# Kernel tuning notes

Measured on AMD Instinct MI355X. Metric: run time of the kernel, lower is better.

Reference implementation:

```python
import jax, jax.numpy as jnp
import numpy as np

N = 100000
F_IN = 128
HID = 64
N_CLS = 40
E = 1600000


def gcn_conv(x, src, dst, W, b, n_nodes):
    """PyG GCNConv: add self-loops, symmetric deg^{-1/2} normalization.

    Self-loop contribution handled analytically (norm_ii = 1/deg_i) so we
    never concatenate self-loop edges.
    """
    h = x @ W                                      # [N, out]
    # in-degree including self-loop
    deg = jax.ops.segment_sum(jnp.ones((src.shape[0],), x.dtype), dst,
                              num_segments=n_nodes) + 1.0
    dinv = jax.lax.rsqrt(deg)                      # deg^{-1/2}, [N]
    norm = dinv[src] * dinv[dst]                   # [E]
    msg = h[src] * norm[:, None]                   # [E, out] gather + scale
    agg = jax.ops.segment_sum(msg, dst, num_segments=n_nodes)
    return agg + h * (dinv * dinv)[:, None] + b


def setup_inputs() -> dict:
    key = jax.random.key(0)
    k1, k2, k3, k4, k5, k6 = jax.random.split(key, 6)
    x = jax.random.normal(k1, (N, F_IN), dtype=jnp.float32)
    edge_index = jax.random.randint(k2, (2, E), 0, N, dtype=jnp.int64)
    W1 = jax.random.normal(k3, (F_IN, HID), dtype=jnp.float32) / np.sqrt(F_IN)
    b1 = jnp.zeros((HID,), jnp.float32)
    W2 = jax.random.normal(k4, (HID, N_CLS), dtype=jnp.float32) / np.sqrt(HID)
    b2 = jnp.zeros((N_CLS,), jnp.float32)
    return {"x": x, "edge_index": edge_index, "W1": W1, "b1": b1,
            "W2": W2, "b2": b2}


def reference(x, edge_index, W1, b1, W2, b2):
    src, dst = edge_index[0], edge_index[1]
    h = jax.nn.relu(gcn_conv(x, src, dst, W1, b1, N))
    # dropout p=0.5 is identity at inference (training=False)
    out = gcn_conv(h, src, dst, W2, b2, N)
    return out
```

## Files before the change

kernel.cpp:

```cpp
#include <hip/hip_runtime.h>
#include <hip/hip_fp16.h>
#include <stdint.h>

#define NN    100000
#define FIN   128
#define HIDN  64
#define NCLS  40
#define NE    1600000
#define NBUCK ((NN + 255) / 256)
#define EPB   4096
#define NEB   ((NE + EPB - 1) / EPB)

typedef unsigned int uint32;
typedef __attribute__((ext_vector_type(8))) short short8v;
typedef __attribute__((ext_vector_type(4))) float f32x4;

static __device__ __forceinline__ unsigned short f2bf(float f) {
  uint32 u = __float_as_uint(f);
  u = (u + 0x7fffu + ((u >> 16) & 1u)) >> 16;
  return (unsigned short)u;
}
static __device__ __forceinline__ uint32 pack2(float lo, float hi) {
  return (uint32)f2bf(lo) | ((uint32)f2bf(hi) << 16);
}
static __device__ __forceinline__ float bf_lo(uint32 v) {
  return __uint_as_float(v << 16);
}
static __device__ __forceinline__ float bf_hi(uint32 v) {
  return __uint_as_float(v & 0xFFFF0000u);
}
static __device__ __forceinline__ float2 h2f2(uint32 w) {
  __half2 h = __builtin_bit_cast(__half2, w);
  return __half22float2(h);
}
static __device__ __forceinline__ f32x4 mfma_bf16(uint4 a, uint4 b, f32x4 c) {
  short8v av = __builtin_bit_cast(short8v, a);
  short8v bv = __builtin_bit_cast(short8v, b);
  return __builtin_amdgcn_mfma_f32_16x16x32_bf16(av, bv, c, 0, 0, 0);
}

static __device__ __forceinline__ int perm_col(int z) {
  return 4 * (z >> 3) + ((z & 7) >> 1) + 16 * (z & 1) + ((z >= 32) ? 16 : 0);
}

#define ACC8(v)                                                              \
  do {                                                                       \
    a[0] += bf_lo((v).x); a[1] += bf_hi((v).x);                              \
    a[2] += bf_lo((v).y); a[3] += bf_hi((v).y);                              \
    a[4] += bf_lo((v).z); a[5] += bf_hi((v).z);                              \
    a[6] += bf_lo((v).w); a[7] += bf_hi((v).w);                              \
  } while (0)

#define ACC8H(v)                                                             \
  do {                                                                       \
    float2 f0 = h2f2((v).x), f1 = h2f2((v).y);                               \
    float2 f2 = h2f2((v).z), f3 = h2f2((v).w);                               \
    a[0] += f0.x; a[1] += f0.y; a[2] += f1.x; a[3] += f1.y;                  \
    a[4] += f2.x; a[5] += f2.y; a[6] += f3.x; a[7] += f3.y;                  \
  } while (0)

__global__ __launch_bounds__(64) void wfrag_kernel(const float* __restrict__ W,
                                                   const float* __restrict__ b1,
                                                   const float* __restrict__ W2,
                                                   const unsigned int* __restrict__ raw,
                                                   uint4* __restrict__ wfrag,
                                                   uint4* __restrict__ w2frag,
                                                   float* __restrict__ b1p,
                                                   int* __restrict__ flag) {
  int bk = blockIdx.x;
  int tid = threadIdx.x;
  if (bk < 32) {
    int idx = bk * 64 + tid;
    int lane = idx & 63;
    int nr = (idx >> 6) & 3;
    int kr = (idx >> 8) & 3;
    int t  = idx >> 10;
    int n  = nr * 16 + (lane & 15);
    int k0 = kr * 32 + (lane >> 4) * 8;
    uint32 w[4];
#pragma unroll
    for (int j = 0; j < 4; ++j) {
      float a = W[(k0 + 2 * j) * HIDN + n];
      float b = W[(k0 + 2 * j + 1) * HIDN + n];
      uint32 ha = f2bf(a), hb = f2bf(b);
      if (t == 0) {
        w[j] = ha | (hb << 16);
      } else {
        float ra = a - __uint_as_float(ha << 16);
        float rb = b - __uint_as_float(hb << 16);
        w[j] = (uint32)f2bf(ra) | ((uint32)f2bf(rb) << 16);
      }
    }
    wfrag[idx] = make_uint4(w[0], w[1], w[2], w[3]);
  } else if (bk < 44) {
    int f = bk - 32;
    int t2 = f / 6;
    int kr = (f / 3) % 2;
    int nf = f % 3;
    int c  = nf * 16 + (tid & 15);
    int k0 = kr * 32 + (tid >> 4) * 8;
    uint32 w[4];
#pragma unroll
    for (int j = 0; j < 4; ++j) {
      float a = (c < NCLS) ? W2[perm_col(k0 + 2 * j) * NCLS + c] : 0.f;
      float b = (c < NCLS) ? W2[perm_col(k0 + 2 * j + 1) * NCLS + c] : 0.f;
      uint32 ha = f2bf(a), hb = f2bf(b);
      if (t2 == 0) {
        w[j] = ha | (hb << 16);
      } else {
        float ra = a - __uint_as_float(ha << 16);
        float rb = b - __uint_as_float(hb << 16);
        w[j] = (uint32)f2bf(ra) | ((uint32)f2bf(rb) << 16);
      }
    }
    w2frag[f * 64 + tid] = make_uint4(w[0], w[1], w[2], w[3]);
  } else {
    b1p[tid] = b1[perm_col(tid)];
    if (tid == 0) {
      int is64 = 1;
      for (int i = 0; i < 64; ++i)
        if (raw[2 * i + 1] != 0u) { is64 = 0; break; }
      *flag = is64;
    }
  }
}

__global__ __launch_bounds__(256) void passA_kernel(const void* __restrict__ eptr,
                                                    const int* __restrict__ flag,
                                                    int* __restrict__ mat) {
  __shared__ int cnt[NBUCK];
  int tid = threadIdx.x;
  for (int i = tid; i < NBUCK; i += 256) cnt[i] = 0;
  __syncthreads();
  int is64 = *flag;
  int base = blockIdx.x * EPB;
#pragma unroll
  for (int k = 0; k < EPB / 256; ++k) {
    int e = base + k * 256 + tid;
    if (e < NE) {
      int d = is64 ? (int)((const long long*)eptr)[e + NE]
                   : ((const int*)eptr)[e + NE];
      atomicAdd(&cnt[d >> 8], 1);
    }
  }
  __syncthreads();
  for (int i = tid; i < NBUCK; i += 256)
    mat[blockIdx.x * NBUCK + i] = cnt[i];
}

__global__ __launch_bounds__(512) void passB1_kernel(int* __restrict__ mat,
                                                     int* __restrict__ tot) {
  __shared__ int s[512];
  int b = blockIdx.x;
  int t = threadIdx.x;
  int v = (t < NEB) ? mat[t * NBUCK + b] : 0;
  s[t] = v;
  __syncthreads();
#pragma unroll
  for (int d = 1; d < 512; d <<= 1) {
    int u = (t >= d) ? s[t - d] : 0;
    __syncthreads();
    s[t] += u;
    __syncthreads();
  }
  if (t < NEB) mat[t * NBUCK + b] = s[t] - v;
  if (t == 511) tot[b] = s[511];
}

__global__ __launch_bounds__(512) void passB2_kernel(const int* __restrict__ tot,
                                                     int* __restrict__ bbase) {
  __shared__ int s[512];
  int i = threadIdx.x;
  int v = (i < NBUCK) ? tot[i] : 0;
  s[i] = v;
  __syncthreads();
#pragma unroll
  for (int d = 1; d < 512; d <<= 1) {
    int u = (i >= d) ? s[i - d] : 0;
    __syncthreads();
    s[i] += u;
    __syncthreads();
  }
  if (i < NBUCK) bbase[i] = s[i] - v;
  if (i == 511) bbase[NBUCK] = s[511];
}

__global__ __launch_bounds__(256) void passC_kernel(const void* __restrict__ eptr,
                                                    const int* __restrict__ flag,
                                                    const int* __restrict__ mat,
                                                    const int* __restrict__ bbase,
                                                    uint32* __restrict__ bbuf) {
  __shared__ int cur[NBUCK];
  int tid = threadIdx.x;
  for (int i = tid; i < NBUCK; i += 256)
    cur[i] = bbase[i] + mat[blockIdx.x * NBUCK + i];
  __syncthreads();
  int is64 = *flag;
  int base = blockIdx.x * EPB;
#pragma unroll
  for (int k = 0; k < EPB / 256; ++k) {
    int e = base + k * 256 + tid;
    if (e < NE) {
      int s, d;
      if (is64) {
        const long long* p = (const long long*)eptr;
        s = (int)p[e]; d = (int)p[e + NE];
      } else {
        const int* p = (const int*)eptr;
        s = p[e]; d = p[e + NE];
      }
      int slot = atomicAdd(&cur[d >> 8], 1);
      bbuf[slot] = (uint32)s | ((uint32)(d & 255) << 17);
    }
  }
}

__global__ __launch_bounds__(256) void build_kernel(const int* __restrict__ bbase,
                                                    const uint32* __restrict__ bbuf,
                                                    int* __restrict__ off,
                                                    float* __restrict__ dinv,
                                                    int* __restrict__ s_src) {
  __shared__ int hist[256];
  __shared__ int lofs[256];
  __shared__ int rank[256];
  int b = blockIdx.x, tid = threadIdx.x;
  int base = bbase[b];
  int count = bbase[b + 1] - base;
  const uint32* p = bbuf + base;
  hist[tid] = 0;
  __syncthreads();
  for (int i = tid; i < count; i += 256) atomicAdd(&hist[p[i] >> 17], 1);
  __syncthreads();
  int deg = hist[tid];
  lofs[tid] = deg;
  __syncthreads();
#pragma unroll
  for (int dd = 1; dd < 256; dd <<= 1) {
    int t = (tid >= dd) ? lofs[tid - dd] : 0;
    __syncthreads();
    lofs[tid] += t;
    __syncthreads();
  }
  int excl = lofs[tid] - deg;
  __syncthreads();
  lofs[tid] = excl;
  rank[tid] = 0;
  int n = b * 256 + tid;
  if (n < NN) {
    off[n] = base + excl;
    dinv[n] = rsqrtf((float)deg + 1.0f);
  }
  if (b == 0 && tid == 0) off[NN] = NE;
  __syncthreads();
  for (int i = tid; i < count; i += 256) {
    uint32 v = p[i];
    int dl = (int)(v >> 17);
    int s = (int)(v & 0x1FFFFu);
    int r = atomicAdd(&rank[dl], 1);
    s_src[base + lofs[dl] + r] = s;
  }
}

__global__ __launch_bounds__(256) void gemm1_kernel(const float* __restrict__ x,
                                                    const uint4* __restrict__ wfrag,
                                                    const float* __restrict__ dinv,
                                                    uint32* __restrict__ hs) {
  int wid = blockIdx.x * 4 + (threadIdx.x >> 6);
  if (wid >= NN / 32) return;
  int lane = threadIdx.x & 63;
  int l15 = lane & 15, lg = lane >> 4;
  int r0 = wid * 32;
  f32x4 acc[2][4];
#pragma unroll
  for (int mr = 0; mr < 2; ++mr)
#pragma unroll
    for (int nr = 0; nr < 4; ++nr) acc[mr][nr] = (f32x4)0.f;
  const float4* x4 = (const float4*)x;
#pragma unroll
  for (int kr = 0; kr < 4; ++kr) {
    uint4 ah[2], al[2];
#pragma unroll
    for (int mr = 0; mr < 2; ++mr) {
      int m = r0 + mr * 16 + l15;
      int q0 = m * 32 + kr * 8 + lg * 2;
      float4 u = x4[q0], v = x4[q0 + 1];
      float xs[8] = {u.x, u.y, u.z, u.w, v.x, v.y, v.z, v.w};
      uint32 hw[4], lw[4];
#pragma unroll
      for (int j = 0; j < 4; ++j) {
        float a0 = xs[2 * j], a1 = xs[2 * j + 1];
        uint32 h0 = f2bf(a0), h1 = f2bf(a1);
        float ra = a0 - __uint_as_float(h0 << 16);
        float rb = a1 - __uint_as_float(h1 << 16);
        hw[j] = h0 | (h1 << 16);
        lw[j] = (uint32)f2bf(ra) | ((uint32)f2bf(rb) << 16);
      }
      ah[mr] = make_uint4(hw[0], hw[1], hw[2], hw[3]);
      al[mr] = make_uint4(lw[0], lw[1], lw[2], lw[3]);
    }
#pragma unroll
    for (int nr = 0; nr < 4; ++nr) {
      uint4 bh = wfrag[(kr * 4 + nr) * 64 + lane];
      uint4 bl = wfrag[((4 + kr) * 4 + nr) * 64 + lane];
#pragma unroll
      for (int mr = 0; mr < 2; ++mr) {
        acc[mr][nr] = mfma_bf16(ah[mr], bh, acc[mr][nr]);
        acc[mr][nr] = mfma_bf16(al[mr], bh, acc[mr][nr]);
        acc[mr][nr] = mfma_bf16(ah[mr], bl, acc[mr][nr]);
      }
    }
  }
#pragma unroll
  for (int mr = 0; mr < 2; ++mr) {
    int rb = r0 + mr * 16 + 4 * lg;
    float4 dv = *(const float4*)&dinv[rb];
#pragma unroll
    for (int a = 0; a < 2; ++a) {
#pragma unroll
      for (int j = 0; j < 4; ++j) {
        float d = (&dv.x)[j];
        uint32 wv = pack2(acc[mr][2 * a][j] * d, acc[mr][2 * a + 1][j] * d);
        hs[(size_t)(rb + j) * 32 + a * 16 + l15] = wv;
      }
    }
  }
}

__global__ __launch_bounds__(256) void agg1_kernel(const int* __restrict__ off,
                                                   const int* __restrict__ s_src,
                                                   const uint4* __restrict__ hs4,
                                                   const float* __restrict__ dinv,
                                                   const float* __restrict__ b1p,
                                                   uint4* __restrict__ g) {
  int tid = threadIdx.x;
  int n = blockIdx.x * 32 + (tid >> 3);
  int hc = tid & 7;
  int j0 = off[n], j1 = off[n + 1];
  float a[8];
  {
    uint4 v = hs4[(size_t)n * 8 + hc];
    a[0] = bf_lo(v.x); a[1] = bf_hi(v.x); a[2] = bf_lo(v.y); a[3] = bf_hi(v.y);
    a[4] = bf_lo(v.z); a[5] = bf_hi(v.z); a[6] = bf_lo(v.w); a[7] = bf_hi(v.w);
  }
  int j = j0;
  for (; j + 3 < j1; j += 4) {
    int s0 = s_src[j], s1 = s_src[j + 1], s2 = s_src[j + 2], s3 = s_src[j + 3];
    uint4 v0 = hs4[(size_t)s0 * 8 + hc];
    uint4 v1 = hs4[(size_t)s1 * 8 + hc];
    uint4 v2 = hs4[(size_t)s2 * 8 + hc];
    uint4 v3 = hs4[(size_t)s3 * 8 + hc];
    ACC8(v0); ACC8(v1); ACC8(v2); ACC8(v3);
  }
  for (; j < j1; ++j) {
    uint4 v0 = hs4[(size_t)s_src[j] * 8 + hc];
    ACC8(v0);
  }
  float di = dinv[n];
  float4 b0 = *(const float4*)&b1p[hc * 8];
  float4 b4 = *(const float4*)&b1p[hc * 8 + 4];
  float r0 = di * fmaxf(a[0] * di + b0.x, 0.f);
  float r1 = di * fmaxf(a[1] * di + b0.y, 0.f);
  float r2 = di * fmaxf(a[2] * di + b0.z, 0.f);
  float r3 = di * fmaxf(a[3] * di + b0.w, 0.f);
  float r4 = di * fmaxf(a[4] * di + b4.x, 0.f);
  float r5 = di * fmaxf(a[5] * di + b4.y, 0.f);
  float r6 = di * fmaxf(a[6] * di + b4.z, 0.f);
  float r7 = di * fmaxf(a[7] * di + b4.w, 0.f);
  uint4 o;
  o.x = pack2(r0, r1); o.y = pack2(r2, r3);
  o.z = pack2(r4, r5); o.w = pack2(r6, r7);
  g[(size_t)n * 8 + hc] = o;
}

__global__ __launch_bounds__(256) void gemm2_kernel(const uint4* __restrict__ g4,
                                                    const uint4* __restrict__ w2frag,
                                                    unsigned short* __restrict__ y16) {
  int wid = blockIdx.x * 4 + (threadIdx.x >> 6);
  if (wid >= NN / 32) return;
  int lane = threadIdx.x & 63;
  int l15 = lane & 15, lg = lane >> 4;
  int r0 = wid * 32;
  f32x4 acc[2][3];
#pragma unroll
  for (int mr = 0; mr < 2; ++mr)
#pragma unroll
    for (int nf = 0; nf < 3; ++nf) acc[mr][nf] = (f32x4)0.f;
#pragma unroll
  for (int kr = 0; kr < 2; ++kr) {
    uint4 a0 = g4[(size_t)(r0 + l15) * 8 + kr * 4 + lg];
    uint4 a1 = g4[(size_t)(r0 + 16 + l15) * 8 + kr * 4 + lg];
#pragma unroll
    for (int nf = 0; nf < 3; ++nf) {
      uint4 bh = w2frag[(kr * 3 + nf) * 64 + lane];
      uint4 bl = w2frag[((2 + kr) * 3 + nf) * 64 + lane];
      acc[0][nf] = mfma_bf16(a0, bh, acc[0][nf]);
      acc[0][nf] = mfma_bf16(a0, bl, acc[0][nf]);
      acc[1][nf] = mfma_bf16(a1, bh, acc[1][nf]);
      acc[1][nf] = mfma_bf16(a1, bl, acc[1][nf]);
    }
  }
#pragma unroll
  for (int mr = 0; mr < 2; ++mr) {
#pragma unroll
    for (int nf = 0; nf < 3; ++nf) {
      int col = nf * 16 + l15;
      if (col < NCLS) {
#pragma unroll
        for (int j = 0; j < 4; ++j) {
          int row = r0 + mr * 16 + 4 * lg + j;
          __half h = __float2half(acc[mr][nf][j]);
          y16[(size_t)row * NCLS + col] = __builtin_bit_cast(unsigned short, h);
        }
      }
    }
  }
}

__global__ __launch_bounds__(256) void agg2y_kernel(const int* __restrict__ off,
                                                    const int* __restrict__ s_src,
                                                    const uint4* __restrict__ y4,
                                                    const float* __restrict__ dinv,
                                                    const float* __restrict__ b2,
                                                    float* __restrict__ out) {
  int T = blockIdx.x * 256 + threadIdx.x;
  int n = T / 5;
  int sub = T - n * 5;
  if (n >= NN) return;
  int j0 = off[n], j1 = off[n + 1];
  float a[8];
  {
    uint4 v = y4[(size_t)n * 5 + sub];
    float2 f0 = h2f2(v.x), f1 = h2f2(v.y), f2 = h2f2(v.z), f3 = h2f2(v.w);
    a[0] = f0.x; a[1] = f0.y; a[2] = f1.x; a[3] = f1.y;
    a[4] = f2.x; a[5] = f2.y; a[6] = f3.x; a[7] = f3.y;
  }
  int j = j0;
  for (; j + 3 < j1; j += 4) {
    int s0 = s_src[j], s1 = s_src[j + 1], s2 = s_src[j + 2], s3 = s_src[j + 3];
    uint4 v0 = y4[(size_t)s0 * 5 + sub];
    uint4 v1 = y4[(size_t)s1 * 5 + sub];
    uint4 v2 = y4[(size_t)s2 * 5 + sub];
    uint4 v3 = y4[(size_t)s3 * 5 + sub];
    ACC8H(v0); ACC8H(v1); ACC8H(v2); ACC8H(v3);
  }
  for (; j < j1; ++j) {
    uint4 v0 = y4[(size_t)s_src[j] * 5 + sub];
    ACC8H(v0);
  }
  float di = dinv[n];
  int c0 = sub * 8;
  float4 bb0 = *(const float4*)&b2[c0];
  float4 bb1 = *(const float4*)&b2[c0 + 4];
  float* op = &out[(size_t)n * NCLS + c0];
  *(float4*)op = make_float4(a[0] * di + bb0.x, a[1] * di + bb0.y,
                             a[2] * di + bb0.z, a[3] * di + bb0.w);
  *(float4*)(op + 4) = make_float4(a[4] * di + bb1.x, a[5] * di + bb1.y,
                                   a[6] * di + bb1.z, a[7] * di + bb1.w);
}

extern "C" void kernel_launch(void* const* d_in, const int* in_sizes, int n_in,
                              void* d_out, int out_size, void* d_ws, size_t ws_size,
                              hipStream_t stream) {
  const float* x  = (const float*)d_in[0];
  const void*  ei = d_in[1];
  const float* W1 = (const float*)d_in[2];
  const float* b1 = (const float*)d_in[3];
  const float* W2 = (const float*)d_in[4];
  const float* b2 = (const float*)d_in[5];
  float* out = (float*)d_out;

  char* w = (char*)d_ws;
  size_t off_b = 0;
  auto carve = [&](size_t bytes) -> void* {
    void* p = w + off_b;
    off_b = (off_b + bytes + 255) & ~(size_t)255;
    return p;
  };
  int*    mat    = (int*)   carve((size_t)NEB * NBUCK * 4);
  int*    tot    = (int*)   carve((size_t)NBUCK * 4);
  int*    bbase  = (int*)   carve((size_t)(NBUCK + 1) * 4);
  int*    offs   = (int*)   carve((size_t)(NN + 1) * 4);
  float*  dinv   = (float*) carve((size_t)NN * 4);
  int*    flag   = (int*)   carve(256);
  int*    s_src  = (int*)   carve((size_t)NE * 4);
  uint32* hs     = (uint32*)carve((size_t)NN * 32 * 4);
  uint4*  g      = (uint4*) carve((size_t)NN * 8 * 16);
  uint32* bbuf   = (uint32*)carve((size_t)NE * 4);
  uint4*  wfrag  = (uint4*) carve((size_t)2048 * 16);
  uint4*  w2frag = (uint4*) carve((size_t)768 * 16);
  float*  b1p    = (float*) carve((size_t)HIDN * 4);
  unsigned short* y16 = (unsigned short*)carve((size_t)NN * NCLS * 2);

  wfrag_kernel<<<45, 64, 0, stream>>>(W1, b1, W2, (const unsigned int*)ei,
                                      wfrag, w2frag, b1p, flag);
  passA_kernel<<<NEB, 256, 0, stream>>>(ei, flag, mat);
  passB1_kernel<<<NBUCK, 512, 0, stream>>>(mat, tot);
  passB2_kernel<<<1, 512, 0, stream>>>(tot, bbase);
  passC_kernel<<<NEB, 256, 0, stream>>>(ei, flag, mat, bbase, bbuf);
  build_kernel<<<NBUCK, 256, 0, stream>>>(bbase, bbuf, offs, dinv, s_src);
  gemm1_kernel<<<(NN / 32 + 3) / 4, 256, 0, stream>>>(x, wfrag, dinv, hs);
  agg1_kernel<<<NN / 32, 256, 0, stream>>>(offs, s_src, (const uint4*)hs, dinv, b1p, g);
  gemm2_kernel<<<(NN / 32 + 3) / 4, 256, 0, stream>>>(g, w2frag, y16);
  agg2y_kernel<<<(NN * 5 + 255) / 256, 256, 0, stream>>>(offs, s_src,
                                                         (const uint4*)y16, dinv, b2, out);
}
```

Before: 229.7 us.

## Fuse CSR build passes into one persistent kernel with grid barriers

Merges the five CSR construction kernels (bucket count, two scans, scatter, per-bucket sort) into a single kernel of NEB=391 blocks separated by software grid-wide barriers on an atomic counter reset by the weight-prep kernel. The goal is to remove four kernel launch gaps and tail effects in the short preprocessing phase. It relies on all 391 blocks being co-resident (true on a 256-CU GPU, but not guaranteed), and it serializes the single-block bucket scan behind a barrier that every block spins on.

Result: slower. 471.8 us (+105.4%).

```diff
diff --git a/kernel.cpp b/kernel.cpp
--- a/kernel.cpp
+++ b/kernel.cpp
@@ -66,7 +66,8 @@
                                                    uint4* __restrict__ wfrag,
                                                    uint4* __restrict__ w2frag,
                                                    float* __restrict__ b1p,
-                                                   int* __restrict__ flag) {
+                                                   int* __restrict__ flag,
+                                                   int* __restrict__ gbar) {
   int bk = blockIdx.x;
   int tid = threadIdx.x;
   if (bk < 32) {
@@ -121,82 +122,99 @@
       for (int i = 0; i < 64; ++i)
         if (raw[2 * i + 1] != 0u) { is64 = 0; break; }
       *flag = is64;
-    }
-  }
-}
-
-__global__ __launch_bounds__(256) void passA_kernel(const void* __restrict__ eptr,
-                                                    const int* __restrict__ flag,
-                                                    int* __restrict__ mat) {
-  __shared__ int cnt[NBUCK];
-  int tid = threadIdx.x;
-  for (int i = tid; i < NBUCK; i += 256) cnt[i] = 0;
+      *gbar = 0;
+    }
+  }
+}
+
+#define GRID_BAR(PH)                                                         \
+  do {                                                                       \
+    __syncthreads();                                                         \
+    if (threadIdx.x == 0) {                                                  \
+      __threadfence();                                                       \
+      __hip_atomic_fetch_add(gbar, 1, __ATOMIC_RELEASE,                      \
+                             __HIP_MEMORY_SCOPE_AGENT);                      \
+      while (__hip_atomic_load(gbar, __ATOMIC_ACQUIRE,                       \
+                               __HIP_MEMORY_SCOPE_AGENT) < NEB * (PH))       \
+        __builtin_amdgcn_s_sleep(2);                                         \
+      __threadfence();                                                       \
+    }                                                                        \
+    __syncthreads();                                                         \
+  } while (0)
+
+__global__ __launch_bounds__(256) void csr_kernel(const void* __restrict__ eptr,
+                                                  const int* __restrict__ flag,
+                                                  int* __restrict__ mat,
+                                                  int* __restrict__ tot,
+                                                  int* __restrict__ bbase,
+                                                  int* __restrict__ off,
+                                                  float* __restrict__ dinv,
+                                                  int* __restrict__ s_src,
+                                                  uint32* __restrict__ bbuf,
+                                                  int* __restrict__ gbar) {
+  __shared__ int smem[1024];
+  int b = blockIdx.x, tid = threadIdx.x;
+  int is64 = *flag;
+  int base = b * EPB;
+
+  for (int i = tid; i < NBUCK; i += 256) smem[i] = 0;
   __syncthreads();
-  int is64 = *flag;
-  int base = blockIdx.x * EPB;
 #pragma unroll
   for (int k = 0; k < EPB / 256; ++k) {
     int e = base + k * 256 + tid;
     if (e < NE) {
       int d = is64 ? (int)((const long long*)eptr)[e + NE]
                    : ((const int*)eptr)[e + NE];
-      atomicAdd(&cnt[d >> 8], 1);
+      atomicAdd(&smem[d >> 8], 1);
     }
   }
   __syncthreads();
+  for (int i = tid; i < NBUCK; i += 256) mat[b * NBUCK + i] = smem[i];
+  GRID_BAR(1);
+
+  {
+    int e0 = 2 * tid, e1 = 2 * tid + 1;
+    int va = (e0 < NEB) ? mat[e0 * NBUCK + b] : 0;
+    int vb = (e1 < NEB) ? mat[e1 * NBUCK + b] : 0;
+    smem[tid] = va + vb;
+    __syncthreads();
+#pragma unroll
+    for (int d = 1; d < 256; d <<= 1) {
+      int u = (tid >= d) ? smem[tid - d] : 0;
+      __syncthreads();
+      smem[tid] += u;
+      __syncthreads();
+    }
+    int P = smem[tid] - (va + vb);
+    if (e0 < NEB) mat[e0 * NBUCK + b] = P;
+    if (e1 < NEB) mat[e1 * NBUCK + b] = P + va;
+    if (tid == 255) tot[b] = smem[255];
+  }
+  GRID_BAR(2);
+
+  if (b == 0) {
+    int e0 = 2 * tid, e1 = 2 * tid + 1;
+    int va = (e0 < NBUCK) ? tot[e0] : 0;
+    int vb = (e1 < NBUCK) ? tot[e1] : 0;
+    smem[tid] = va + vb;
+    __syncthreads();
+#pragma unroll
+    for (int d = 1; d < 256; d <<= 1) {
+      int u = (tid >= d) ? smem[tid - d] : 0;
+      __syncthreads();
+      smem[tid] += u;
+      __syncthreads();
+    }
+    int P = smem[tid] - (va + vb);
+    if (e0 < NBUCK) bbase[e0] = P;
+    if (e1 < NBUCK) bbase[e1] = P + va;
+    if (tid == 255) bbase[NBUCK] = smem[255];
+  }
+  GRID_BAR(3);
+
   for (int i = tid; i < NBUCK; i += 256)
-    mat[blockIdx.x * NBUCK + i] = cnt[i];
-}
-
-__global__ __launch_bounds__(512) void passB1_kernel(int* __restrict__ mat,
-                                                     int* __restrict__ tot) {
-  __shared__ int s[512];
-  int b = blockIdx.x;
-  int t = threadIdx.x;
-  int v = (t < NEB) ? mat[t * NBUCK + b] : 0;
-  s[t] = v;
+    smem[i] = bbase[i] + mat[b * NBUCK + i];
   __syncthreads();
-#pragma unroll
-  for (int d = 1; d < 512; d <<= 1) {
-    int u = (t >= d) ? s[t - d] : 0;
-    __syncthreads();
-    s[t] += u;
-    __syncthreads();
-  }
-  if (t < NEB) mat[t * NBUCK + b] = s[t] - v;
-  if (t == 511) tot[b] = s[511];
-}
-
-__global__ __launch_bounds__(512) void passB2_kernel(const int* __restrict__ tot,
-                                                     int* __restrict__ bbase) {
-  __shared__ int s[512];
-  int i = threadIdx.x;
-  int v = (i < NBUCK) ? tot[i] : 0;
-  s[i] = v;
-  __syncthreads();
-#pragma unroll
-  for (int d = 1; d < 512; d <<= 1) {
-    int u = (i >= d) ? s[i - d] : 0;
-    __syncthreads();
-    s[i] += u;
-    __syncthreads();
-  }
-  if (i < NBUCK) bbase[i] = s[i] - v;
-  if (i == 511) bbase[NBUCK] = s[511];
-}
-
-__global__ __launch_bounds__(256) void passC_kernel(const void* __restrict__ eptr,
-                                                    const int* __restrict__ flag,
-                                                    const int* __restrict__ mat,
-                                                    const int* __restrict__ bbase,
-                                                    uint32* __restrict__ bbuf) {
-  __shared__ int cur[NBUCK];
-  int tid = threadIdx.x;
-  for (int i = tid; i < NBUCK; i += 256)
-    cur[i] = bbase[i] + mat[blockIdx.x * NBUCK + i];
-  __syncthreads();
-  int is64 = *flag;
-  int base = blockIdx.x * EPB;
 #pragma unroll
   for (int k = 0; k < EPB / 256; ++k) {
     int e = base + k * 256 + tid;
@@ -209,55 +227,51 @@
         const int* p = (const int*)eptr;
         s = p[e]; d = p[e + NE];
       }
-      int slot = atomicAdd(&cur[d >> 8], 1);
+      int slot = atomicAdd(&smem[d >> 8], 1);
       bbuf[slot] = (uint32)s | ((uint32)(d & 255) << 17);
     }
   }
-}
-
-__global__ __launch_bounds__(256) void build_kernel(const int* __restrict__ bbase,
-                                                    const uint32* __restrict__ bbuf,
-                                                    int* __restrict__ off,
-                                                    float* __restrict__ dinv,
-                                                    int* __restrict__ s_src) {
-  __shared__ int hist[256];
-  __shared__ int lofs[256];
-  __shared__ int rank[256];
-  int b = blockIdx.x, tid = threadIdx.x;
-  int base = bbase[b];
-  int count = bbase[b + 1] - base;
-  const uint32* p = bbuf + base;
-  hist[tid] = 0;
-  __syncthreads();
-  for (int i = tid; i < count; i += 256) atomicAdd(&hist[p[i] >> 17], 1);
-  __syncthreads();
-  int deg = hist[tid];
-  lofs[tid] = deg;
-  __syncthreads();
-#pragma unroll
-  for (int dd = 1; dd < 256; dd <<= 1) {
-    int t = (tid >= dd) ? lofs[tid - dd] : 0;
-    __syncthreads();
-    lofs[tid] += t;
-    __syncthreads();
-  }
-  int excl = lofs[tid] - deg;
-  __syncthreads();
-  lofs[tid] = excl;
-  rank[tid] = 0;
-  int n = b * 256 + tid;
-  if (n < NN) {
-    off[n] = base + excl;
-    dinv[n] = rsqrtf((float)deg + 1.0f);
-  }
-  if (b == 0 && tid == 0) off[NN] = NE;
-  __syncthreads();
-  for (int i = tid; i < count; i += 256) {
-    uint32 v = p[i];
-    int dl = (int)(v >> 17);
-    int s = (int)(v & 0x1FFFFu);
-    int r = atomicAdd(&rank[dl], 1);
-    s_src[base + lofs[dl] + r] = s;
+  GRID_BAR(4);
+
+  {
+    int* hist = smem;
+    int* lofs = smem + 256;
+    int* rank = smem + 512;
+    int bb = bbase[b];
+    int count = bbase[b + 1] - bb;
+    const uint32* p = bbuf + bb;
+    hist[tid] = 0;
+    __syncthreads();
+    for (int i = tid; i < count; i += 256) atomicAdd(&hist[p[i] >> 17], 1);
+    __syncthreads();
+    int deg = hist[tid];
+    lofs[tid] = deg;
+    __syncthreads();
+#pragma unroll
+    for (int dd = 1; dd < 256; dd <<= 1) {
+      int t2 = (tid >= dd) ? lofs[tid - dd] : 0;
+      __syncthreads();
+      lofs[tid] += t2;
+      __syncthreads();
+    }
+    int excl = lofs[tid] - deg;
+    __syncthreads();
+    lofs[tid] = excl;
+    rank[tid] = 0;
+    int n = b * 256 + tid;
+    if (n < NN) {
+      off[n] = bb + excl;
+      dinv[n] = rsqrtf((float)deg + 1.0f);
+    }
+    if (b == 0 && tid == 0) off[NN] = NE;
+    __syncthreads();
+    for (int i = tid; i < count; i += 256) {
+      uint32 v = p[i];
+      int dl = (int)(v >> 17);
+      int s = (int)(v & 0x1FFFFu);
+      int r = atomicAdd(&rank[dl], 1);
+      s_src[bb + lofs[dl] + r] = s;
+    }
   }
 }
 
@@ -482,6 +496,7 @@
   int*    offs   = (int*)   carve((size_t)(NN + 1) * 4);
   float*  dinv   = (float*) carve((size_t)NN * 4);
   int*    flag   = (int*)   carve(256);
+  int*    gbar   = (int*)   carve(256);
   int*    s_src  = (int*)   carve((size_t)NE * 4);
   uint32* hs     = (uint32*)carve((size_t)NN * 32 * 4);
   uint4*  g      = (uint4*) carve((size_t)NN * 8 * 16);
@@ -492,12 +507,9 @@
   unsigned short* y16 = (unsigned short*)carve((size_t)NN * NCLS * 2);
 
   wfrag_kernel<<<45, 64, 0, stream>>>(W1, b1, W2, (const unsigned int*)ei,
-                                      wfrag, w2frag, b1p, flag);
-  passA_kernel<<<NEB, 256, 0, stream>>>(ei, flag, mat);
-  passB1_kernel<<<NBUCK, 512, 0, stream>>>(mat, tot);
-  passB2_kernel<<<1, 512, 0, stream>>>(tot, bbase);
-  passC_kernel<<<NEB, 256, 0, stream>>>(ei, flag, mat, bbase, bbuf);
-  build_kernel<<<NBUCK, 256, 0, stream>>>(bbase, bbuf, offs, dinv, s_src);
+                                      wfrag, w2frag, b1p, flag, gbar);
+  csr_kernel<<<NEB, 256, 0, stream>>>(ei, flag, mat, tot, bbase, offs, dinv,
+                                      s_src, bbuf, gbar);
   gemm1_kernel<<<(NN / 32 + 3) / 4, 256, 0, stream>>>(x, wfrag, dinv, hs);
   agg1_kernel<<<NN / 32, 256, 0, stream>>>(offs, s_src, (const uint4*)hs, dinv, b1p, g);
   gemm2_kernel<<<(NN / 32 + 3) / 4, 256, 0, stream>>>(g, w2frag, y16);
```
